# Performance work log

Hardware: AMD Instinct MI355X
Metric: run time of the kernel (lower is better)

## Reference

```python
import jax, jax.numpy as jnp
import numpy as np

B = 16
H = W = 56
C = 384
WS = 7            # window size
SS = 3            # shift size
NH = 12           # num heads
HD = C // NH      # head dim
N = WS * WS       # tokens per window (49)
NW = (H // WS) * (W // WS)  # windows per image (64)
HID = 4 * C       # MLP hidden
SCALE = HD ** -0.5
EPS = 1e-5


def _rel_pos_index():
    coords = np.stack(np.meshgrid(np.arange(WS), np.arange(WS), indexing='ij')).reshape(2, -1)
    rel = (coords[:, :, None] - coords[:, None, :]).transpose(1, 2, 0)  # [N,N,2]
    rel[:, :, 0] += WS - 1
    rel[:, :, 1] += WS - 1
    rel[:, :, 0] *= 2 * WS - 1
    return rel.sum(-1).astype(np.int32)  # [N,N] in [0, (2WS-1)^2)


def _attn_mask():
    img = np.zeros((H, W))
    cnt = 0
    for hs in (slice(0, -WS), slice(-WS, -SS), slice(-SS, None)):
        for ws in (slice(0, -WS), slice(-WS, -SS), slice(-SS, None)):
            img[hs, ws] = cnt
            cnt += 1
    mw = img.reshape(H // WS, WS, W // WS, WS).transpose(0, 2, 1, 3).reshape(-1, N)  # [NW,N]
    d = mw[:, None, :] - mw[:, :, None]  # [NW,N,N]
    return np.where(d != 0, -100.0, 0.0).astype(np.float32)


def setup_inputs() -> dict:
    key = jax.random.key(0)
    ks = jax.random.split(key, 8)
    std = 0.02
    return {
        'x': jax.random.normal(ks[0], (B, H * W, C), jnp.float32),
        'g1': jnp.ones((C,), jnp.float32),
        'b1': jnp.zeros((C,), jnp.float32),
        'qkv_w': jax.random.normal(ks[1], (C, 3 * C), jnp.float32) * std,
        'qkv_b': jnp.zeros((3 * C,), jnp.float32),
        'rpb_table': jax.random.normal(ks[2], ((2 * WS - 1) ** 2, NH), jnp.float32) * std,
        'proj_w': jax.random.normal(ks[3], (C, C), jnp.float32) * std,
        'proj_b': jnp.zeros((C,), jnp.float32),
        'g2': jnp.ones((C,), jnp.float32),
        'b2': jnp.zeros((C,), jnp.float32),
        'fc1_w': jax.random.normal(ks[4], (C, HID), jnp.float32) * std,
        'fc1_b': jnp.zeros((HID,), jnp.float32),
        'fc2_w': jax.random.normal(ks[5], (HID, C), jnp.float32) * std,
        'fc2_b': jnp.zeros((C,), jnp.float32),
        'rel_idx': jnp.asarray(_rel_pos_index()),
        'attn_mask': jnp.asarray(_attn_mask()),
    }


def _ln(x, g, b):
    m = x.mean(-1, keepdims=True)
    v = ((x - m) ** 2).mean(-1, keepdims=True)
    return (x - m) / jnp.sqrt(v + EPS) * g + b


def reference(x, g1, b1, qkv_w, qkv_b, rpb_table, proj_w, proj_b,
              g2, b2, fc1_w, fc1_b, fc2_w, fc2_b, rel_idx, attn_mask):
    shortcut = x
    h = _ln(x, g1, b1).reshape(B, H, W, C)
    # cyclic shift
    h = jnp.roll(h, (-SS, -SS), axis=(1, 2))
    # window partition -> [B*NW, N, C]
    win = h.reshape(B, H // WS, WS, W // WS, WS, C).transpose(0, 1, 3, 2, 4, 5).reshape(-1, N, C)
    # qkv
    qkv = (win @ qkv_w + qkv_b).reshape(-1, N, 3, NH, HD).transpose(2, 0, 3, 1, 4)
    q, k, v = qkv[0] * SCALE, qkv[1], qkv[2]  # [B*NW, NH, N, HD]
    attn = jnp.einsum('bhnd,bhmd->bhnm', q, k)  # [B*NW, NH, N, N]
    # relative position bias
    rpb = rpb_table[rel_idx.reshape(-1)].reshape(N, N, NH).transpose(2, 0, 1)  # [NH,N,N]
    attn = attn + rpb[None]
    # shifted-window attention mask
    attn = attn.reshape(B, NW, NH, N, N) + attn_mask[None, :, None]
    attn = jax.nn.softmax(attn.reshape(-1, NH, N, N), axis=-1)
    out = jnp.einsum('bhnm,bhmd->bhnd', attn, v).transpose(0, 2, 1, 3).reshape(-1, N, C)
    out = out @ proj_w + proj_b
    # window reverse + reverse shift
    out = out.reshape(B, H // WS, W // WS, WS, WS, C).transpose(0, 1, 3, 2, 4, 5).reshape(B, H, W, C)
    out = jnp.roll(out, (SS, SS), axis=(1, 2)).reshape(B, H * W, C)
    x = shortcut + out
    # MLP (exact GELU, as nn.GELU default)
    h2 = _ln(x, g2, b2)
    h2 = jax.nn.gelu(h2 @ fc1_w + fc1_b, approximate=False) @ fc2_w + fc2_b
    return x + h2
```

## Files before the change

kernel.cpp:

```cpp
#include <hip/hip_runtime.h>
#include <hip/hip_bf16.h>
#include <math.h>

typedef __hip_bfloat16 bf16;
typedef __attribute__((ext_vector_type(8))) short short8;
typedef __attribute__((ext_vector_type(4))) float f32x4;

#define C_DIM 384
#define SS 3
#define SCALE_ATTN 0.17677669529663687f
#define LN_EPS 1e-5f

typedef const __attribute__((address_space(1))) void g_cvoid;
typedef __attribute__((address_space(3))) void l_void;
__device__ __forceinline__ void gl_lds16(const void* g, void* l) {
    __builtin_amdgcn_global_load_lds((g_cvoid*)g, (l_void*)l, 16, 0, 0);
}

__global__ void transpose_cast_kernel(const float* __restrict__ in, bf16* __restrict__ out,
                                      int R, int Cc) {
    int idx = blockIdx.x * 256 + threadIdx.x;
    if (idx < R * Cc) {
        int r = idx / Cc, c = idx - r * Cc;
        out[(size_t)c * R + r] = __float2bfloat16(in[idx]);
    }
}

__global__ void build_bm_kernel(const float* __restrict__ rpb, const int* __restrict__ rel_idx,
                                const float* __restrict__ mask, float* __restrict__ BM) {
    int idx = blockIdx.x * 256 + threadIdx.x;
    int col = idx & 63, row = (idx >> 6) & 63;
    int h = (idx >> 12) % 12, wi = idx / (12 * 4096);
    float v = -1e30f;
    if (row < 49 && col < 49)
        v = rpb[rel_idx[row * 49 + col] * 12 + h] + mask[(size_t)wi * 2401 + row * 49 + col];
    BM[idx] = v;
}

__global__ __launch_bounds__(256)
void ln1_shift_window(const float* __restrict__ x, const float* __restrict__ g,
                      const float* __restrict__ bta, bf16* __restrict__ win) {
    int wave = threadIdx.x >> 6, lane = threadIdx.x & 63;
    int token = blockIdx.x * 4 + wave;
    int bw = token / 49, ntk = token - bw * 49;
    int bb = bw >> 6, wi = bw & 63;
    int wh = wi >> 3, wwi = wi & 7;
    int rr = ntk / 7, cc = ntk - rr * 7;
    int hs = wh * 7 + rr + SS; if (hs >= 56) hs -= 56;
    int ws = wwi * 7 + cc + SS; if (ws >= 56) ws -= 56;
    const float* src = x + ((size_t)(bb * 3136 + hs * 56 + ws)) * C_DIM;

    float v[6]; float s = 0.f, sq = 0.f;
    #pragma unroll
    for (int j = 0; j < 6; j++) {
        v[j] = src[lane + j * 64];
        s += v[j]; sq += v[j] * v[j];
    }
    #pragma unroll
    for (int o = 32; o > 0; o >>= 1) { s += __shfl_xor(s, o, 64); sq += __shfl_xor(sq, o, 64); }
    float mean = s * (1.0f / 384.0f);
    float var  = sq * (1.0f / 384.0f) - mean * mean;
    float rstd = rsqrtf(var + LN_EPS);

    bf16* dst = win + (size_t)token * C_DIM;
    #pragma unroll
    for (int j = 0; j < 6; j++) {
        int c = lane + j * 64;
        dst[c] = __float2bfloat16((v[j] - mean) * rstd * g[c] + bta[c]);
    }
}

__global__ __launch_bounds__(256)
void ln2_kernel(const float* __restrict__ xmid, const float* __restrict__ g,
                const float* __restrict__ bta, bf16* __restrict__ out) {
    int wave = threadIdx.x >> 6, lane = threadIdx.x & 63;
    int token = blockIdx.x * 4 + wave;
    const float* src = xmid + (size_t)token * C_DIM;
    float v[6]; float s = 0.f, sq = 0.f;
    #pragma unroll
    for (int j = 0; j < 6; j++) {
        v[j] = src[lane + j * 64];
        s += v[j]; sq += v[j] * v[j];
    }
    #pragma unroll
    for (int o = 32; o > 0; o >>= 1) { s += __shfl_xor(s, o, 64); sq += __shfl_xor(sq, o, 64); }
    float mean = s * (1.0f / 384.0f);
    float var  = sq * (1.0f / 384.0f) - mean * mean;
    float rstd = rsqrtf(var + LN_EPS);
    bf16* dst = out + (size_t)token * C_DIM;
    #pragma unroll
    for (int j = 0; j < 6; j++) {
        int c = lane + j * 64;
        dst[c] = __float2bfloat16((v[j] - mean) * rstd * g[c] + bta[c]);
    }
}

template <int MODE>
__global__ __launch_bounds__(256)
void gemm_kernel(const bf16* __restrict__ A, const bf16* __restrict__ BT,
                 const float* __restrict__ bias, void* __restrict__ out,
                 const float* __restrict__ resid, int M, int N, int K) {
    __shared__ bf16 As[2][8192];
    __shared__ bf16 Bs[2][8192];

    int tid = threadIdx.x;
    int wave = tid >> 6, lane = tid & 63, quad = lane >> 4, r = lane & 15;
    int wave_m = wave & 1, wave_n = wave >> 1;

    int nN = N >> 7;
    int nwg = gridDim.x;
    int bid = blockIdx.x;
    int q8 = nwg >> 3, r8 = nwg & 7;
    int xcd = bid & 7, loc = bid >> 3;
    int swz = (xcd < r8 ? xcd * (q8 + 1) : r8 * (q8 + 1) + (xcd - r8) * q8) + loc;
    int mtile = swz / nN;
    int ntile = swz - mtile * nN;
    int m0 = mtile << 7, n0 = ntile << 7;

    f32x4 acc[4][4] = {};

    auto stage = [&](int buf, int k0) {
        #pragma unroll
        for (int c = 0; c < 4; c++) {
            int slot = c * 256 + wave * 64 + lane;
            int panel = slot >> 7, row = slot & 127;
            gl_lds16(A + (size_t)(m0 + row) * K + k0 + panel * 8,
                     &As[buf][(c * 256 + wave * 64) * 8]);
            gl_lds16(BT + (size_t)(n0 + row) * K + k0 + panel * 8,
                     &Bs[buf][(c * 256 + wave * 64) * 8]);
        }
    };

    auto compute = [&](int buf) {
        #pragma unroll
        for (int ks = 0; ks < 2; ks++) {
            int pq = ks * 4 + quad;
            short8 a[4], b[4];
            #pragma unroll
            for (int mt = 0; mt < 4; mt++)
                a[mt] = *(const short8*)&As[buf][(pq * 128 + wave_m * 64 + mt * 16 + r) * 8];
            #pragma unroll
            for (int nt = 0; nt < 4; nt++)
                b[nt] = *(const short8*)&Bs[buf][(pq * 128 + wave_n * 64 + nt * 16 + r) * 8];
            #pragma unroll
            for (int mt = 0; mt < 4; mt++)
                #pragma unroll
                for (int nt = 0; nt < 4; nt++)
                    acc[mt][nt] = __builtin_amdgcn_mfma_f32_16x16x32_bf16(
                        a[mt], b[nt], acc[mt][nt], 0, 0, 0);
        }
    };

    stage(0, 0);
    __syncthreads();

    int nk = K >> 6;
    int cur = 0;
    for (int kt = 0; kt < nk - 1; kt++) {
        stage(cur ^ 1, (kt + 1) << 6);
        compute(cur);
        __syncthreads();
        cur ^= 1;
    }
    compute(cur);

    #pragma unroll
    for (int mt = 0; mt < 4; mt++) {
        #pragma unroll
        for (int nt = 0; nt < 4; nt++) {
            int n = n0 + wave_n * 64 + nt * 16 + r;
            float bv = bias[n];
            #pragma unroll
            for (int reg = 0; reg < 4; reg++) {
                int m = m0 + wave_m * 64 + mt * 16 + quad * 4 + reg;
                float v = acc[mt][nt][reg] + bv;
                if (MODE == 0) {
                    ((bf16*)out)[(size_t)m * N + n] = __float2bfloat16(v);
                } else if (MODE == 1) {
                    float gl = 0.5f * v * (1.0f + erff(v * 0.70710678118654752f));
                    ((bf16*)out)[(size_t)m * N + n] = __float2bfloat16(gl);
                } else if (MODE == 2) {
                    int bw = m / 49, ntk = m - bw * 49;
                    int bb = bw >> 6, wi = bw & 63;
                    int wh = wi >> 3, wwi = wi & 7;
                    int rr = ntk / 7, cc = ntk - rr * 7;
                    int ho = wh * 7 + rr + SS; if (ho >= 56) ho -= 56;
                    int wo = wwi * 7 + cc + SS; if (wo >= 56) wo -= 56;
                    size_t dst = ((size_t)(bb * 3136 + ho * 56 + wo)) * C_DIM + n;
                    ((float*)out)[dst] = v + resid[dst];
                } else {
                    size_t idx = (size_t)m * N + n;
                    ((float*)out)[idx] = v + resid[idx];
                }
            }
        }
    }
}

__global__ __launch_bounds__(256)
void attn_mfma_kernel(const bf16* __restrict__ qkv, const float* __restrict__ BM,
                      bf16* __restrict__ out) {
    __shared__ bf16 P_lds[4][4096];
    __shared__ bf16 V_lds[4][2048];
    int wave = threadIdx.x >> 6, lane = threadIdx.x & 63;
    int quad = lane >> 4, m16 = lane & 15;
    int bw = blockIdx.x;
    int h = blockIdx.y * 4 + wave;
    int wi = bw & 63;

    const bf16* base = qkv + (size_t)bw * 49 * 1152 + h * 32;

    bf16* Vt = V_lds[wave];
    #pragma unroll
    for (int it = 0; it < 16; it++) {
        int idx = it * 64 + lane;
        int n = idx >> 4, dp = idx & 15;
        int d0 = dp * 2;
        unsigned val = 0;
        if (n < 49)
            val = *(const unsigned*)(base + (size_t)n * 1152 + 768 + d0);
        bf16 v0 = ((const bf16*)&val)[0], v1 = ((const bf16*)&val)[1];
        int cb = (n & 56);
        Vt[d0 * 64 + ((cb ^ ((d0 & 7) << 3)) | (n & 7))] = v0;
        int d1 = d0 + 1;
        Vt[d1 * 64 + ((cb ^ ((d1 & 7) << 3)) | (n & 7))] = v1;
    }

    short8 qf[4], kf[4];
    #pragma unroll
    for (int t = 0; t < 4; t++) {
        int row = t * 16 + m16;
        int rc = (row < 49) ? row : 0;
        qf[t] = *(const short8*)(base + (size_t)rc * 1152 + quad * 8);
        kf[t] = *(const short8*)(base + (size_t)rc * 1152 + 384 + quad * 8);
    }
    f32x4 S[4][4] = {};
    #pragma unroll
    for (int mt = 0; mt < 4; mt++)
        #pragma unroll
        for (int nt = 0; nt < 4; nt++)
            S[mt][nt] = __builtin_amdgcn_mfma_f32_16x16x32_bf16(qf[mt], kf[nt], S[mt][nt], 0, 0, 0);

    const float* bmw = BM + (((size_t)wi * 12 + h) << 12);
    bf16* Pw = P_lds[wave];
    #pragma unroll
    for (int mt = 0; mt < 4; mt++) {
        #pragma unroll
        for (int reg = 0; reg < 4; reg++) {
            int row = mt * 16 + quad * 4 + reg;
            float p[4];
            float mx = -1e30f;
            #pragma unroll
            for (int nt = 0; nt < 4; nt++) {
                int col = nt * 16 + m16;
                float s = S[mt][nt][reg] * SCALE_ATTN + bmw[row * 64 + col];
                p[nt] = s;
                mx = fmaxf(mx, s);
            }
            #pragma unroll
            for (int o = 1; o < 16; o <<= 1) mx = fmaxf(mx, __shfl_xor(mx, o, 64));
            float sm = 0.f;
            #pragma unroll
            for (int nt = 0; nt < 4; nt++) { p[nt] = __expf(p[nt] - mx); sm += p[nt]; }
            #pragma unroll
            for (int o = 1; o < 16; o <<= 1) sm += __shfl_xor(sm, o, 64);
            float inv = 1.0f / sm;
            int r7 = (row & 7) << 3;
            #pragma unroll
            for (int nt = 0; nt < 4; nt++) {
                int col = nt * 16 + m16;
                int sw = ((col & 56) ^ r7) | (col & 7);
                Pw[row * 64 + sw] = __float2bfloat16(p[nt] * inv);
            }
        }
    }

    f32x4 O[4][2] = {};
    #pragma unroll
    for (int ks = 0; ks < 2; ks++) {
        int chunk = ks * 4 + quad;
        short8 pa[4], vb[2];
        #pragma unroll
        for (int mt = 0; mt < 4; mt++) {
            int row = mt * 16 + m16;
            pa[mt] = *(const short8*)&Pw[row * 64 + ((chunk ^ (row & 7)) << 3)];
        }
        #pragma unroll
        for (int nt = 0; nt < 2; nt++) {
            int d = nt * 16 + m16;
            vb[nt] = *(const short8*)&Vt[d * 64 + ((chunk ^ (d & 7)) << 3)];
        }
        #pragma unroll
        for (int mt = 0; mt < 4; mt++)
            #pragma unroll
            for (int nt = 0; nt < 2; nt++)
                O[mt][nt] = __builtin_amdgcn_mfma_f32_16x16x32_bf16(pa[mt], vb[nt], O[mt][nt], 0, 0, 0);
    }

    bf16* orow = out + (size_t)bw * 49 * 384 + h * 32;
    #pragma unroll
    for (int mt = 0; mt < 4; mt++) {
        #pragma unroll
        for (int reg = 0; reg < 4; reg++) {
            int row = mt * 16 + quad * 4 + reg;
            if (row < 49) {
                #pragma unroll
                for (int nt = 0; nt < 2; nt++)
                    orow[(size_t)row * 384 + nt * 16 + m16] = __float2bfloat16(O[mt][nt][reg]);
            }
        }
    }
}

extern "C" void kernel_launch(void* const* d_in, const int* in_sizes, int n_in,
                              void* d_out, int out_size, void* d_ws, size_t ws_size,
                              hipStream_t stream) {
    const float* x      = (const float*)d_in[0];
    const float* g1     = (const float*)d_in[1];
    const float* b1     = (const float*)d_in[2];
    const float* qkv_w  = (const float*)d_in[3];
    const float* qkv_b  = (const float*)d_in[4];
    const float* rpb    = (const float*)d_in[5];
    const float* proj_w = (const float*)d_in[6];
    const float* proj_b = (const float*)d_in[7];
    const float* g2     = (const float*)d_in[8];
    const float* b2     = (const float*)d_in[9];
    const float* fc1_w  = (const float*)d_in[10];
    const float* fc1_b  = (const float*)d_in[11];
    const float* fc2_w  = (const float*)d_in[12];
    const float* fc2_b  = (const float*)d_in[13];
    const int*   rel_idx   = (const int*)d_in[14];
    const float* attn_mask = (const float*)d_in[15];

    const int M = 50176;

    char* ws = (char*)d_ws;
    size_t off = 0;
    bf16* bufA   = (bf16*)(ws + off); off += (size_t)M * 384 * 2;
    bf16* bufBC  = (bf16*)(ws + off); off += (size_t)M * 1536 * 2;
    float* xmid  = (float*)(ws + off); off += (size_t)M * 384 * 4;
    bf16* qkv_wT  = (bf16*)(ws + off); off += (size_t)1152 * 384 * 2;
    bf16* proj_wT = (bf16*)(ws + off); off += (size_t)384 * 384 * 2;
    bf16* fc1_wT  = (bf16*)(ws + off); off += (size_t)1536 * 384 * 2;
    bf16* fc2_wT  = (bf16*)(ws + off); off += (size_t)384 * 1536 * 2;
    float* BM = (float*)(bufBC + (size_t)M * 1152);

    build_bm_kernel<<<64 * 12 * 4096 / 256, 256, 0, stream>>>(rpb, rel_idx, attn_mask, BM);

    transpose_cast_kernel<<<(384 * 1152 + 255) / 256, 256, 0, stream>>>(qkv_w, qkv_wT, 384, 1152);
    transpose_cast_kernel<<<(384 * 384 + 255) / 256, 256, 0, stream>>>(proj_w, proj_wT, 384, 384);
    transpose_cast_kernel<<<(384 * 1536 + 255) / 256, 256, 0, stream>>>(fc1_w, fc1_wT, 384, 1536);
    transpose_cast_kernel<<<(1536 * 384 + 255) / 256, 256, 0, stream>>>(fc2_w, fc2_wT, 1536, 384);

    ln1_shift_window<<<M / 4, 256, 0, stream>>>(x, g1, b1, bufA);

    gemm_kernel<0><<<(M / 128) * (1152 / 128), 256, 0, stream>>>(
        bufA, qkv_wT, qkv_b, bufBC, nullptr, M, 1152, 384);

    attn_mfma_kernel<<<dim3(1024, 3), 256, 0, stream>>>(bufBC, BM, bufA);

    gemm_kernel<2><<<(M / 128) * (384 / 128), 256, 0, stream>>>(
        bufA, proj_wT, proj_b, xmid, x, M, 384, 384);

    ln2_kernel<<<M / 4, 256, 0, stream>>>(xmid, g2, b2, bufA);

    gemm_kernel<1><<<(M / 128) * (1536 / 128), 256, 0, stream>>>(
        bufA, fc1_wT, fc1_b, bufBC, nullptr, M, 1536, 384);

    gemm_kernel<3><<<(M / 128) * (384 / 128), 256, 0, stream>>>(
        bufBC, fc2_wT, fc2_b, d_out, xmid, M, 384, 1536);
}
```

Before: 795.2 us.

## Replace LDS-staged GEMM tiles with direct global-to-register double-buffered loads

The GEMM kernel no longer stages A and B tiles through shared memory with global_load_lds and barriers. Each wave now loads its own MFMA operand fragments straight from global memory into two register buffers, alternating between them so loads overlap the MFMA work. s_setprio is raised around the MFMA blocks. This removes LDS traffic and block-wide syncs, but waves that share rows now fetch duplicate data through the caches. It also raises register pressure and uses short 64-byte row segments per load.

```diff
diff --git a/kernel.cpp b/kernel.cpp
--- a/kernel.cpp
+++ b/kernel.cpp
@@ -10,12 +10,6 @@
 #define SS 3
 #define SCALE_ATTN 0.17677669529663687f
 #define LN_EPS 1e-5f
-
-typedef const __attribute__((address_space(1))) void g_cvoid;
-typedef __attribute__((address_space(3))) void l_void;
-__device__ __forceinline__ void gl_lds16(const void* g, void* l) {
-    __builtin_amdgcn_global_load_lds((g_cvoid*)g, (l_void*)l, 16, 0, 0);
-}
 
 __global__ void transpose_cast_kernel(const float* __restrict__ in, bf16* __restrict__ out,
                                       int R, int Cc) {
@@ -100,9 +94,6 @@
 void gemm_kernel(const bf16* __restrict__ A, const bf16* __restrict__ BT,
                  const float* __restrict__ bias, void* __restrict__ out,
                  const float* __restrict__ resid, int M, int N, int K) {
-    __shared__ bf16 As[2][8192];
-    __shared__ bf16 Bs[2][8192];
-
     int tid = threadIdx.x;
     int wave = tid >> 6, lane = tid & 63, quad = lane >> 4, r = lane & 15;
     int wave_m = wave & 1, wave_n = wave >> 1;
@@ -117,52 +108,46 @@
     int ntile = swz - mtile * nN;
     int m0 = mtile << 7, n0 = ntile << 7;
 
+    const bf16* Ap = A  + (size_t)(m0 + wave_m * 64 + r) * K + quad * 8;
+    const bf16* Bp = BT + (size_t)(n0 + wave_n * 64 + r) * K + quad * 8;
+
     f32x4 acc[4][4] = {};
-
-    auto stage = [&](int buf, int k0) {
-        #pragma unroll
-        for (int c = 0; c < 4; c++) {
-            int slot = c * 256 + wave * 64 + lane;
-            int panel = slot >> 7, row = slot & 127;
-            gl_lds16(A + (size_t)(m0 + row) * K + k0 + panel * 8,
-                     &As[buf][(c * 256 + wave * 64) * 8]);
-            gl_lds16(BT + (size_t)(n0 + row) * K + k0 + panel * 8,
-                     &Bs[buf][(c * 256 + wave * 64) * 8]);
-        }
-    };
-
-    auto compute = [&](int buf) {
-        #pragma unroll
-        for (int ks = 0; ks < 2; ks++) {
-            int pq = ks * 4 + quad;
-            short8 a[4], b[4];
-            #pragma unroll
-            for (int mt = 0; mt < 4; mt++)
-                a[mt] = *(const short8*)&As[buf][(pq * 128 + wave_m * 64 + mt * 16 + r) * 8];
-            #pragma unroll
-            for (int nt = 0; nt < 4; nt++)
-                b[nt] = *(const short8*)&Bs[buf][(pq * 128 + wave_n * 64 + nt * 16 + r) * 8];
-            #pragma unroll
-            for (int mt = 0; mt < 4; mt++)
-                #pragma unroll
-                for (int nt = 0; nt < 4; nt++)
-                    acc[mt][nt] = __builtin_amdgcn_mfma_f32_16x16x32_bf16(
-                        a[mt], b[nt], acc[mt][nt], 0, 0, 0);
-        }
-    };
-
-    stage(0, 0);
-    __syncthreads();
-
-    int nk = K >> 6;
-    int cur = 0;
-    for (int kt = 0; kt < nk - 1; kt++) {
-        stage(cur ^ 1, (kt + 1) << 6);
-        compute(cur);
-        __syncthreads();
-        cur ^= 1;
-    }
-    compute(cur);
+    short8 a0[4][2], a1[4][2], b0[4][2], b1[4][2];
+
+    #define LOADF(AS, BS, k0)                                                  \
+        _Pragma("unroll")                                                      \
+        for (int mt = 0; mt < 4; mt++) {                                       \
+            AS[mt][0] = *(const short8*)(Ap + (size_t)(mt * 16) * K + (k0));   \
+            AS[mt][1] = *(const short8*)(Ap + (size_t)(mt * 16) * K + (k0) + 32); \
+        }                                                                      \
+        _Pragma("unroll")                                                      \
+        for (int nt = 0; nt < 4; nt++) {                                       \
+            BS[nt][0] = *(const short8*)(Bp + (size_t)(nt * 16) * K + (k0));   \
+            BS[nt][1] = *(const short8*)(Bp + (size_t)(nt * 16) * K + (k0) + 32); \
+        }
+
+    #define MMF(AS, BS)                                                        \
+        __builtin_amdgcn_s_setprio(1);                                         \
+        _Pragma("unroll")                                                      \
+        for (int ks = 0; ks < 2; ks++)                                         \
+            _Pragma("unroll")                                                  \
+            for (int mt = 0; mt < 4; mt++)                                     \
+                _Pragma("unroll")                                              \
+                for (int nt = 0; nt < 4; nt++)                                 \
+                    acc[mt][nt] = __builtin_amdgcn_mfma_f32_16x16x32_bf16(     \
+                        AS[mt][ks], BS[nt][ks], acc[mt][nt], 0, 0, 0);         \
+        __builtin_amdgcn_s_setprio(0);
+
+    LOADF(a0, b0, 0)
+    for (int k = 64; k < K; k += 128) {
+        LOADF(a1, b1, k)
+        MMF(a0, b0)
+        int kn = (k + 64 < K) ? (k + 64) : 0;
+        LOADF(a0, b0, kn)
+        MMF(a1, b1)
+    }
+    #undef LOADF
+    #undef MMF
 
     #pragma unroll
     for (int mt = 0; mt < 4; mt++) {
@@ -343,6 +328,7 @@
     bf16* proj_wT = (bf16*)(ws + off); off += (size_t)384 * 384 * 2;
     bf16* fc1_wT  = (bf16*)(ws + off); off += (size_t)1536 * 384 * 2;
     bf16* fc2_wT  = (bf16*)(ws + off); off += (size_t)384 * 1536 * 2;
+    off += 4096;
     float* BM = (float*)(bufBC + (size_t)M * 1152);
 
     build_bm_kernel<<<64 * 12 * 4096 / 256, 256, 0, stream>>>(rpb, rel_idx, attn_mask, BM);
```

Measured after the change: 1.111 ms. +39.7%, slower.

## Use triple-buffered K=32 stages with explicit vmcnt waits in GEMM

Applied to the files above, without the earlier changes.

Changes the GEMM main loop from double-buffered K=64 tiles to triple-buffered K=32 tiles, prefetching two stages ahead. Plain __syncthreads is replaced by partial s_waitcnt vmcnt plus raw barriers, so loads for later stages can stay in flight while the current tile is computed. The MFMA block is wrapped in s_setprio to favour the matrix issue. The cost is twice as many barrier iterations per K. The hand-written waitcnt counts also assume a fixed number of outstanding loads per stage, which the code must keep consistent.

```diff
diff --git a/kernel.cpp b/kernel.cpp
--- a/kernel.cpp
+++ b/kernel.cpp
@@ -100,8 +100,8 @@
 void gemm_kernel(const bf16* __restrict__ A, const bf16* __restrict__ BT,
                  const float* __restrict__ bias, void* __restrict__ out,
                  const float* __restrict__ resid, int M, int N, int K) {
-    __shared__ bf16 As[2][8192];
-    __shared__ bf16 Bs[2][8192];
+    __shared__ bf16 As[3][4096];
+    __shared__ bf16 Bs[3][4096];
 
     int tid = threadIdx.x;
     int wave = tid >> 6, lane = tid & 63, quad = lane >> 4, r = lane & 15;
@@ -121,7 +121,7 @@
 
     auto stage = [&](int buf, int k0) {
         #pragma unroll
-        for (int c = 0; c < 4; c++) {
+        for (int c = 0; c < 2; c++) {
             int slot = c * 256 + wave * 64 + lane;
             int panel = slot >> 7, row = slot & 127;
             gl_lds16(A + (size_t)(m0 + row) * K + k0 + panel * 8,
@@ -132,37 +132,46 @@
     };
 
     auto compute = [&](int buf) {
-        #pragma unroll
-        for (int ks = 0; ks < 2; ks++) {
-            int pq = ks * 4 + quad;
-            short8 a[4], b[4];
-            #pragma unroll
-            for (int mt = 0; mt < 4; mt++)
-                a[mt] = *(const short8*)&As[buf][(pq * 128 + wave_m * 64 + mt * 16 + r) * 8];
+        short8 a[4], b[4];
+        #pragma unroll
+        for (int mt = 0; mt < 4; mt++)
+            a[mt] = *(const short8*)&As[buf][(quad * 128 + wave_m * 64 + mt * 16 + r) * 8];
+        #pragma unroll
+        for (int nt = 0; nt < 4; nt++)
+            b[nt] = *(const short8*)&Bs[buf][(quad * 128 + wave_n * 64 + nt * 16 + r) * 8];
+        __builtin_amdgcn_s_setprio(1);
+        #pragma unroll
+        for (int mt = 0; mt < 4; mt++)
             #pragma unroll
             for (int nt = 0; nt < 4; nt++)
-                b[nt] = *(const short8*)&Bs[buf][(pq * 128 + wave_n * 64 + nt * 16 + r) * 8];
-            #pragma unroll
-            for (int mt = 0; mt < 4; mt++)
-                #pragma unroll
-                for (int nt = 0; nt < 4; nt++)
-                    acc[mt][nt] = __builtin_amdgcn_mfma_f32_16x16x32_bf16(
-                        a[mt], b[nt], acc[mt][nt], 0, 0, 0);
-        }
+                acc[mt][nt] = __builtin_amdgcn_mfma_f32_16x16x32_bf16(
+                    a[mt], b[nt], acc[mt][nt], 0, 0, 0);
+        __builtin_amdgcn_s_setprio(0);
     };
 
+    int nk = K >> 5;
+
     stage(0, 0);
-    __syncthreads();
-
-    int nk = K >> 6;
-    int cur = 0;
-    for (int kt = 0; kt < nk - 1; kt++) {
-        stage(cur ^ 1, (kt + 1) << 6);
-        compute(cur);
-        __syncthreads();
-        cur ^= 1;
-    }
-    compute(cur);
+    stage(1, 32);
+    asm volatile("s_waitcnt vmcnt(4)" ::: "memory");
+    __builtin_amdgcn_s_barrier();
+    __builtin_amdgcn_sched_barrier(0);
+
+    int buf = 0;
+    for (int kt = 0; kt < nk; kt++) {
+        int pf = kt + 2;
+        int pbuf = buf + 2; if (pbuf >= 3) pbuf -= 3;
+        if (pf < nk) stage(pbuf, pf << 5);
+        compute(buf);
+        if (kt + 1 < nk) {
+            __builtin_amdgcn_sched_barrier(0);
+            if (pf < nk) asm volatile("s_waitcnt vmcnt(4)" ::: "memory");
+            else         asm volatile("s_waitcnt vmcnt(0)" ::: "memory");
+            __builtin_amdgcn_s_barrier();
+            __builtin_amdgcn_sched_barrier(0);
+        }
+        buf++; if (buf == 3) buf = 0;
+    }
 
     #pragma unroll
     for (int mt = 0; mt < 4; mt++) {
```

New measurement: 774.4 us. 1.03x faster.

## Load GEMM B operand directly into registers, double-buffered, bypassing LDS

Applied to the files above, without the earlier changes.

The B tile is no longer staged through shared memory. Each wave loads its own B fragments straight from global memory into registers, double-buffered across two k-steps. The main loop is unrolled by two with fixed buffers, and s_setprio is raised around the MFMA block. This halves LDS traffic and footprint, which may allow higher occupancy. In exchange, B reads are duplicated across the two wave_m waves, more registers are used, and K must now be a multiple of 128.

```diff
diff --git a/kernel.cpp b/kernel.cpp
--- a/kernel.cpp
+++ b/kernel.cpp
@@ -101,7 +101,6 @@
                  const float* __restrict__ bias, void* __restrict__ out,
                  const float* __restrict__ resid, int M, int N, int K) {
     __shared__ bf16 As[2][8192];
-    __shared__ bf16 Bs[2][8192];
 
     int tid = threadIdx.x;
     int wave = tid >> 6, lane = tid & 63, quad = lane >> 4, r = lane & 15;
@@ -117,7 +116,10 @@
     int ntile = swz - mtile * nN;
     int m0 = mtile << 7, n0 = ntile << 7;
 
+    const bf16* Bp = BT + (size_t)(n0 + wave_n * 64 + r) * K + quad * 8;
+
     f32x4 acc[4][4] = {};
+    short8 b0[4][2], b1[4][2];
 
     auto stage = [&](int buf, int k0) {
         #pragma unroll
@@ -126,43 +128,50 @@
             int panel = slot >> 7, row = slot & 127;
             gl_lds16(A + (size_t)(m0 + row) * K + k0 + panel * 8,
                      &As[buf][(c * 256 + wave * 64) * 8]);
-            gl_lds16(BT + (size_t)(n0 + row) * K + k0 + panel * 8,
-                     &Bs[buf][(c * 256 + wave * 64) * 8]);
         }
     };
 
-    auto compute = [&](int buf) {
+    #define LOADB(BS, k0)                                                       \
+        _Pragma("unroll")                                                       \
+        for (int nt = 0; nt < 4; nt++) {                                        \
+            BS[nt][0] = *(const short8*)(Bp + (size_t)(nt * 16) * K + (k0));    \
+            BS[nt][1] = *(const short8*)(Bp + (size_t)(nt * 16) * K + (k0) + 32); \
+        }
+
+    auto compute = [&](int buf, short8 (&b)[4][2]) {
         #pragma unroll
         for (int ks = 0; ks < 2; ks++) {
             int pq = ks * 4 + quad;
-            short8 a[4], b[4];
+            short8 a[4];
             #pragma unroll
             for (int mt = 0; mt < 4; mt++)
                 a[mt] = *(const short8*)&As[buf][(pq * 128 + wave_m * 64 + mt * 16 + r) * 8];
-            #pragma unroll
-            for (int nt = 0; nt < 4; nt++)
-                b[nt] = *(const short8*)&Bs[buf][(pq * 128 + wave_n * 64 + nt * 16 + r) * 8];
+            __builtin_amdgcn_s_setprio(1);
             #pragma unroll
             for (int mt = 0; mt < 4; mt++)
                 #pragma unroll
                 for (int nt = 0; nt < 4; nt++)
                     acc[mt][nt] = __builtin_amdgcn_mfma_f32_16x16x32_bf16(
-                        a[mt], b[nt], acc[mt][nt], 0, 0, 0);
+                        a[mt], b[nt][ks], acc[mt][nt], 0, 0, 0);
+            __builtin_amdgcn_s_setprio(0);
         }
     };
 
     stage(0, 0);
+    LOADB(b0, 0)
     __syncthreads();
 
-    int nk = K >> 6;
-    int cur = 0;
-    for (int kt = 0; kt < nk - 1; kt++) {
-        stage(cur ^ 1, (kt + 1) << 6);
-        compute(cur);
+    int np = K >> 7;
+    for (int p = 0; p < np; p++) {
+        int k = p << 7;
+        stage(1, k + 64); LOADB(b1, k + 64)
+        compute(0, b0);
         __syncthreads();
-        cur ^= 1;
-    }
-    compute(cur);
+        if (p + 1 < np) { stage(0, k + 128); LOADB(b0, k + 128) }
+        compute(1, b1);
+        __syncthreads();
+    }
+    #undef LOADB
 
     #pragma unroll
     for (int mt = 0; mt < 4; mt++) {
```

Result: slower. 854.9 us (+7.5%).
